# Kernel optimization log

Measured on AMD Instinct MI355X. Metric: run time of the kernel, lower is better.

Reference implementation:

```python
import jax, jax.numpy as jnp
import numpy as np

N_USERS = 50000
N_ENTITIES = 100000
D = 64
R = 16
E_UI = 1500000
E_KG = 100000


def setup_inputs() -> dict:
    key = jax.random.key(0)
    ks = jax.random.split(key, 7)
    s = 1.0 / np.sqrt(D)  # ~xavier scale
    return {
        "user_indices": jnp.arange(N_USERS, dtype=jnp.int32),
        "item_indices": jnp.arange(N_ENTITIES, dtype=jnp.int32),
        "edge_index_ui": jax.random.randint(ks[0], (2, E_UI), 0, N_USERS + N_ENTITIES, dtype=jnp.int32),
        "edge_index_kg": jax.random.randint(ks[1], (2, E_KG), 0, N_ENTITIES, dtype=jnp.int32),
        "edge_type_kg": jax.random.randint(ks[2], (E_KG,), 0, R, dtype=jnp.int32),
        "user_table": (jax.random.normal(ks[3], (N_USERS, D)) * s).astype(jnp.float32),
        "entity_table": (jax.random.normal(ks[4], (N_ENTITIES, D)) * s).astype(jnp.float32),
        "W": (jax.random.normal(ks[5], (D, D)) * s).astype(jnp.float32),
        "W_r": (jax.random.normal(ks[6], (R, D, D)) * s).astype(jnp.float32),
    }


def _kgat_layer(x, edge_index, W, W_r, edge_type=None):
    # PyG aggr='add', flow source_to_target: x_j = x[src], x_i = x[dst], scatter to dst
    src, dst = edge_index[0], edge_index[1]
    x_j = x[src]  # [E, D]
    x_i = x[dst]  # [E, D]
    if edge_type is None:
        x_j_t = x_j @ W  # [E, D]
    else:
        # per-edge relation-specific transform: bmm(x_j[:,None,:], W_r[edge_type])
        x_j_t = jnp.einsum('ed,edo->eo', x_j, W_r[edge_type])
    # bi-interaction attention
    x_i_t = x_i @ W
    logits = jnp.sum(x_i_t * x_j_t, axis=1, keepdims=True)  # [E, 1]
    logits = jax.nn.leaky_relu(logits, negative_slope=0.2)
    scores = jax.nn.softmax(logits, axis=0)  # GLOBAL softmax over all edges (as in source)
    msg = scores * x_j_t  # [E, D]
    return jax.ops.segment_sum(msg, dst, num_segments=x.shape[0])


def reference(user_indices, item_indices, edge_index_ui, edge_index_kg, edge_type_kg,
              user_table, entity_table, W, W_r):
    user_embeds = user_table[user_indices]      # [n_users, D]
    item_embeds = entity_table[item_indices]    # [n_entities, D]
    x = jnp.concatenate([user_embeds, item_embeds], axis=0)
    # single layer (layer_dims = [embed_dim])
    x_ui = _kgat_layer(x, edge_index_ui, W, W_r, edge_type=None)
    x_kg = _kgat_layer(item_embeds, edge_index_kg, W, W_r, edge_type=edge_type_kg)
    x = x.at[N_USERS:].add(x_kg)  # faithful to source: overwritten by next line (dead store)
    x = jax.nn.relu(x_ui)
    # F.dropout(training=False) -> identity in eval mode
    return (x[:N_USERS], x[N_USERS:])
```

## Files before the change

kernel.cpp:

```cpp
#include <hip/hip_runtime.h>

#define NU 50000
#define NE 100000
#define NN 150000
#define DD 64
#define EUI 1500000

#define TPB 256
#define NBLK 2048
#define NXB 2344
#define NXH (NXB + NBLK)
#define NBF2 9375
#define NSC 9375

#define XWB_OFF    0ull
#define CNT_OFF    4800000ull
#define PSUM_OFF   4950000ull
#define SCAL_OFF   4959375ull

__device__ __forceinline__ unsigned bfpack(float a, float b) {
  unsigned ua = __float_as_uint(a);
  ua = (ua + 0x7fffu + ((ua >> 16) & 1u)) >> 16;
  unsigned ub = __float_as_uint(b);
  ub = (ub + 0x7fffu + ((ub >> 16) & 1u)) & 0xffff0000u;
  return (ua & 0xffffu) | ub;
}

template <int CTRL>
__device__ __forceinline__ float dpp_add(float x) {
  int y = __builtin_amdgcn_update_dpp(0, __float_as_int(x), CTRL, 0xF, 0xF, false);
  return x + __int_as_float(y);
}
__device__ __forceinline__ float row16_sum(float x) {
  x = dpp_add<0x124>(x);
  x = dpp_add<0x128>(x);
  x = dpp_add<0xB1>(x);
  x = dpp_add<0x4E>(x);
  return x;
}

__global__ __launch_bounds__(TPB) void k_xw_hist(const int* __restrict__ uidx,
                                                 const int* __restrict__ iidx,
                                                 const float* __restrict__ ut,
                                                 const float* __restrict__ et,
                                                 const float* __restrict__ W,
                                                 unsigned* __restrict__ xwb,
                                                 const int* __restrict__ ei,
                                                 unsigned* __restrict__ cnt,
                                                 int* __restrict__ ssrcp) {
  const int bi = blockIdx.x;
  int idx;
  bool hist;
  if (bi < 2 * NBLK) { hist = (bi & 1); idx = bi >> 1; }
  else               { hist = false;    idx = bi - NBLK; }

  if (hist) {
    for (int e = idx * TPB + threadIdx.x; e < EUI; e += NBLK * TPB) {
      const int dst = ei[EUI + e];
      const int src = ei[e];
      const unsigned r = atomicAdd(&cnt[dst], 1u);
      if (r < 64u) ssrcp[((size_t)dst << 6) + r] = src;
    }
    return;
  }

  __shared__ float Ws[DD * DD];
  __shared__ float Xs[64 * 68];
  const int t = threadIdx.x;
  {
    const float4* W4 = (const float4*)W;
    float4* Ws4 = (float4*)Ws;
#pragma unroll
    for (int i = 0; i < 4; ++i) Ws4[t + i * TPB] = W4[t + i * TPB];
  }
  {
    const int rl = t >> 2, ch = t & 3;
    int row = idx * 64 + rl;
    if (row >= NN) row = NN - 1;
    const float4* s4 = (const float4*)((row < NU)
        ? ut + (size_t)uidx[row] * DD
        : et + (size_t)iidx[row - NU] * DD);
    float4* x4 = (float4*)(Xs + rl * 68);
#pragma unroll
    for (int j = 0; j < 4; ++j) x4[ch + 4 * j] = s4[ch + 4 * j];
  }
  __syncthreads();
  const int q = t & 15, g = t >> 4;
  float4 acc[4] = {{0,0,0,0},{0,0,0,0},{0,0,0,0},{0,0,0,0}};
  const float* __restrict__ wsq = Ws + 4 * q;
  const float* __restrict__ xsg = Xs + (4 * g) * 68;
#pragma unroll 1
  for (int kc = 0; kc < 16; ++kc) {
    const float4 w0 = *(const float4*)(wsq + (4 * kc + 0) * DD);
    const float4 w1 = *(const float4*)(wsq + (4 * kc + 1) * DD);
    const float4 w2 = *(const float4*)(wsq + (4 * kc + 2) * DD);
    const float4 w3 = *(const float4*)(wsq + (4 * kc + 3) * DD);
#pragma unroll
    for (int i = 0; i < 4; ++i) {
      const float4 x = *(const float4*)(xsg + i * 68 + 4 * kc);
      acc[i].x = fmaf(x.x, w0.x, acc[i].x);
      acc[i].y = fmaf(x.x, w0.y, acc[i].y);
      acc[i].z = fmaf(x.x, w0.z, acc[i].z);
      acc[i].w = fmaf(x.x, w0.w, acc[i].w);
      acc[i].x = fmaf(x.y, w1.x, acc[i].x);
      acc[i].y = fmaf(x.y, w1.y, acc[i].y);
      acc[i].z = fmaf(x.y, w1.z, acc[i].z);
      acc[i].w = fmaf(x.y, w1.w, acc[i].w);
      acc[i].x = fmaf(x.z, w2.x, acc[i].x);
      acc[i].y = fmaf(x.z, w2.y, acc[i].y);
      acc[i].z = fmaf(x.z, w2.z, acc[i].z);
      acc[i].w = fmaf(x.z, w2.w, acc[i].w);
      acc[i].x = fmaf(x.w, w3.x, acc[i].x);
      acc[i].y = fmaf(x.w, w3.y, acc[i].y);
      acc[i].z = fmaf(x.w, w3.z, acc[i].z);
      acc[i].w = fmaf(x.w, w3.w, acc[i].w);
    }
  }
#pragma unroll
  for (int i = 0; i < 4; ++i) {
    const int row = idx * 64 + 4 * g + i;
    if (row < NN) {
      uint2 p;
      p.x = bfpack(acc[i].x, acc[i].y);
      p.y = bfpack(acc[i].z, acc[i].w);
      ((uint2*)(xwb + (size_t)row * 32))[q] = p;
    }
  }
}

__global__ __launch_bounds__(TPB) void k_fused(const unsigned* __restrict__ cnt,
                                               const int* ssrcp,
                                               const unsigned* __restrict__ xwb,
                                               float* out,
                                               float* __restrict__ psum) {
  const int lane = threadIdx.x & 63;
  const int wv = threadIdx.x >> 6;
  const int sub = lane >> 4;
  const int q = lane & 15;
  const int n = blockIdx.x * 16 + wv * 4 + sub;
  const uint2* __restrict__ x2 = (const uint2*)xwb;
  const uint2 dv = x2[(size_t)n * 16 + q];
  const float vd0 = __uint_as_float(dv.x << 16);
  const float vd1 = __uint_as_float(dv.x & 0xffff0000u);
  const float vd2 = __uint_as_float(dv.y << 16);
  const float vd3 = __uint_as_float(dv.y & 0xffff0000u);
  const int deg = min((int)cnt[n], 64);
  const size_t base = (size_t)n << 6;
  float a0 = 0.f, a1 = 0.f, a2 = 0.f, a3 = 0.f, wacc = 0.f;
  for (int it = 0;; it += 2) {
    const bool act0 = it < deg;
    if (!__any(act0)) break;
    const bool act1 = it + 1 < deg;
    int s0 = ssrcp[base + (act0 ? it : 0)];
    int s1 = ssrcp[base + (act1 ? it + 1 : 0)];
    if (!act0) s0 = 0;
    if (!act1) s1 = 0;
    const uint2 sv0 = x2[(size_t)s0 * 16 + q];
    const uint2 sv1 = x2[(size_t)s1 * 16 + q];
    const float u0 = __uint_as_float(sv0.x << 16);
    const float u1 = __uint_as_float(sv0.x & 0xffff0000u);
    const float u2 = __uint_as_float(sv0.y << 16);
    const float u3 = __uint_as_float(sv0.y & 0xffff0000u);
    const float t0 = __uint_as_float(sv1.x << 16);
    const float t1 = __uint_as_float(sv1.x & 0xffff0000u);
    const float t2 = __uint_as_float(sv1.y << 16);
    const float t3 = __uint_as_float(sv1.y & 0xffff0000u);
    float p0 = vd0 * u0;
    p0 = fmaf(vd1, u1, p0);
    p0 = fmaf(vd2, u2, p0);
    p0 = fmaf(vd3, u3, p0);
    float p1 = vd0 * t0;
    p1 = fmaf(vd1, t1, p1);
    p1 = fmaf(vd2, t2, p1);
    p1 = fmaf(vd3, t3, p1);
    p0 = row16_sum(p0);
    p1 = row16_sum(p1);
    const float l0 = (p0 > 0.f) ? p0 : 0.2f * p0;
    const float l1 = (p1 > 0.f) ? p1 : 0.2f * p1;
    float w0 = __expf(l0);
    float w1 = __expf(l1);
    if (!act0) w0 = 0.f;
    if (!act1) w1 = 0.f;
    a0 = fmaf(w0, u0, a0);
    a1 = fmaf(w0, u1, a1);
    a2 = fmaf(w0, u2, a2);
    a3 = fmaf(w0, u3, a3);
    a0 = fmaf(w1, t0, a0);
    a1 = fmaf(w1, t1, a1);
    a2 = fmaf(w1, t2, a2);
    a3 = fmaf(w1, t3, a3);
    wacc += w0 + w1;
  }
  float4 r = {a0, a1, a2, a3};
  ((float4*)(out + (size_t)n * DD))[q] = r;
  __shared__ float sm[16];
  if (q == 0) sm[wv * 4 + sub] = wacc;
  __syncthreads();
  if (threadIdx.x == 0) {
    float s = 0.f;
#pragma unroll
    for (int i = 0; i < 16; ++i) s += sm[i];
    psum[blockIdx.x] = s;
  }
}

__global__ __launch_bounds__(TPB) void k_rsum(const float* __restrict__ psum,
                                              float* __restrict__ scal) {
  float s = 0.f;
  for (int i = threadIdx.x; i < NBF2; i += TPB) s += psum[i];
#pragma unroll
  for (int off = 32; off; off >>= 1) s += __shfl_xor(s, off, 64);
  __shared__ float sm[4];
  if ((threadIdx.x & 63) == 0) sm[threadIdx.x >> 6] = s;
  __syncthreads();
  if (threadIdx.x == 0) scal[0] = sm[0] + sm[1] + sm[2] + sm[3];
}

__global__ __launch_bounds__(TPB) void k_scale(float* __restrict__ out,
                                               const float* __restrict__ scal) {
  const float inv = 1.0f / scal[0];
  const int i = blockIdx.x * TPB + threadIdx.x;
  float4* o4 = (float4*)out;
  float4 v = o4[i];
  v.x = fmaxf(v.x * inv, 0.f);
  v.y = fmaxf(v.y * inv, 0.f);
  v.z = fmaxf(v.z * inv, 0.f);
  v.w = fmaxf(v.w * inv, 0.f);
  o4[i] = v;
}

extern "C" void kernel_launch(void* const* d_in, const int* in_sizes, int n_in,
                              void* d_out, int out_size, void* d_ws, size_t ws_size,
                              hipStream_t stream) {
  const int* uidx = (const int*)d_in[0];
  const int* iidx = (const int*)d_in[1];
  const int* ei_ui = (const int*)d_in[2];
  const float* ut = (const float*)d_in[5];
  const float* et = (const float*)d_in[6];
  const float* W = (const float*)d_in[7];

  float* out = (float*)d_out;
  float* ws = (float*)d_ws;
  unsigned* xwb = (unsigned*)(ws + XWB_OFF);
  unsigned* cnt = (unsigned*)(ws + CNT_OFF);
  float* psum = ws + PSUM_OFF;
  float* scal = ws + SCAL_OFF;
  int* ssrcp = (int*)d_out;

  (void)hipMemsetAsync(cnt, 0, (size_t)NN * sizeof(unsigned), stream);

  k_xw_hist<<<NXH, TPB, 0, stream>>>(uidx, iidx, ut, et, W, xwb, ei_ui, cnt, ssrcp);
  k_fused<<<NBF2, TPB, 0, stream>>>(cnt, ssrcp, xwb, out, psum);
  k_rsum<<<1, TPB, 0, stream>>>(psum, scal);
  k_scale<<<NSC, TPB, 0, stream>>>(out, scal);
}
```

Measured before the change: 255.3 us.

## Fuse aggregation, reduction and scaling into one persistent cooperative kernel

Replaces the three kernels (aggregation, softmax-denominator reduction, scale+ReLU) with one persistent cooperative kernel. Each block loops over tiles, folds its partial sum into a global atomic, waits at a grid-wide sync, then applies the normalisation and ReLU. The neighbour loop now uses a trip count shared by the wave and prefetches the next source indices. This removes two kernel launches and the partial-sum buffer, at the cost of a grid barrier and a fixed grid of 1024 blocks that may limit latency hiding.

```diff
diff --git a/kernel.cpp b/kernel.cpp
--- a/kernel.cpp
+++ b/kernel.cpp
@@ -1,4 +1,5 @@
 #include <hip/hip_runtime.h>
+#include <hip/hip_cooperative_groups.h>
 
 #define NU 50000
 #define NE 100000
@@ -11,12 +12,11 @@
 #define NXB 2344
 #define NXH (NXB + NBLK)
 #define NBF2 9375
-#define NSC 9375
+#define NPERS 1024
 
 #define XWB_OFF    0ull
 #define CNT_OFF    4800000ull
-#define PSUM_OFF   4950000ull
-#define SCAL_OFF   4959375ull
+#define SCAL_OFF   4950000ull
 
 __device__ __forceinline__ unsigned bfpack(float a, float b) {
   unsigned ua = __float_as_uint(a);
@@ -128,105 +128,110 @@
   }
 }
 
-__global__ __launch_bounds__(TPB) void k_fused(const unsigned* __restrict__ cnt,
-                                               const int* ssrcp,
-                                               const unsigned* __restrict__ xwb,
-                                               float* out,
-                                               float* __restrict__ psum) {
+__global__ __launch_bounds__(TPB) void k_fused_all(const unsigned* __restrict__ cnt,
+                                                   const int* ssrcp,
+                                                   const unsigned* __restrict__ xwb,
+                                                   float* out,
+                                                   float* scal) {
   const int lane = threadIdx.x & 63;
   const int wv = threadIdx.x >> 6;
   const int sub = lane >> 4;
   const int q = lane & 15;
-  const int n = blockIdx.x * 16 + wv * 4 + sub;
   const uint2* __restrict__ x2 = (const uint2*)xwb;
-  const uint2 dv = x2[(size_t)n * 16 + q];
-  const float vd0 = __uint_as_float(dv.x << 16);
-  const float vd1 = __uint_as_float(dv.x & 0xffff0000u);
-  const float vd2 = __uint_as_float(dv.y << 16);
-  const float vd3 = __uint_as_float(dv.y & 0xffff0000u);
-  const int deg = min((int)cnt[n], 64);
-  const size_t base = (size_t)n << 6;
-  float a0 = 0.f, a1 = 0.f, a2 = 0.f, a3 = 0.f, wacc = 0.f;
-  for (int it = 0;; it += 2) {
-    const bool act0 = it < deg;
-    if (!__any(act0)) break;
-    const bool act1 = it + 1 < deg;
-    int s0 = ssrcp[base + (act0 ? it : 0)];
-    int s1 = ssrcp[base + (act1 ? it + 1 : 0)];
-    if (!act0) s0 = 0;
-    if (!act1) s1 = 0;
-    const uint2 sv0 = x2[(size_t)s0 * 16 + q];
-    const uint2 sv1 = x2[(size_t)s1 * 16 + q];
-    const float u0 = __uint_as_float(sv0.x << 16);
-    const float u1 = __uint_as_float(sv0.x & 0xffff0000u);
-    const float u2 = __uint_as_float(sv0.y << 16);
-    const float u3 = __uint_as_float(sv0.y & 0xffff0000u);
-    const float t0 = __uint_as_float(sv1.x << 16);
-    const float t1 = __uint_as_float(sv1.x & 0xffff0000u);
-    const float t2 = __uint_as_float(sv1.y << 16);
-    const float t3 = __uint_as_float(sv1.y & 0xffff0000u);
-    float p0 = vd0 * u0;
-    p0 = fmaf(vd1, u1, p0);
-    p0 = fmaf(vd2, u2, p0);
-    p0 = fmaf(vd3, u3, p0);
-    float p1 = vd0 * t0;
-    p1 = fmaf(vd1, t1, p1);
-    p1 = fmaf(vd2, t2, p1);
-    p1 = fmaf(vd3, t3, p1);
-    p0 = row16_sum(p0);
-    p1 = row16_sum(p1);
-    const float l0 = (p0 > 0.f) ? p0 : 0.2f * p0;
-    const float l1 = (p1 > 0.f) ? p1 : 0.2f * p1;
-    float w0 = __expf(l0);
-    float w1 = __expf(l1);
-    if (!act0) w0 = 0.f;
-    if (!act1) w1 = 0.f;
-    a0 = fmaf(w0, u0, a0);
-    a1 = fmaf(w0, u1, a1);
-    a2 = fmaf(w0, u2, a2);
-    a3 = fmaf(w0, u3, a3);
-    a0 = fmaf(w1, t0, a0);
-    a1 = fmaf(w1, t1, a1);
-    a2 = fmaf(w1, t2, a2);
-    a3 = fmaf(w1, t3, a3);
-    wacc += w0 + w1;
-  }
-  float4 r = {a0, a1, a2, a3};
-  ((float4*)(out + (size_t)n * DD))[q] = r;
-  __shared__ float sm[16];
-  if (q == 0) sm[wv * 4 + sub] = wacc;
-  __syncthreads();
-  if (threadIdx.x == 0) {
-    float s = 0.f;
-#pragma unroll
-    for (int i = 0; i < 16; ++i) s += sm[i];
-    psum[blockIdx.x] = s;
-  }
-}
-
-__global__ __launch_bounds__(TPB) void k_rsum(const float* __restrict__ psum,
-                                              float* __restrict__ scal) {
-  float s = 0.f;
-  for (int i = threadIdx.x; i < NBF2; i += TPB) s += psum[i];
+  float wtot = 0.f;
+
+  for (int tile = blockIdx.x; tile < NBF2; tile += NPERS) {
+    const int n = tile * 16 + wv * 4 + sub;
+    const uint2 dv = x2[(size_t)n * 16 + q];
+    const float vd0 = __uint_as_float(dv.x << 16);
+    const float vd1 = __uint_as_float(dv.x & 0xffff0000u);
+    const float vd2 = __uint_as_float(dv.y << 16);
+    const float vd3 = __uint_as_float(dv.y & 0xffff0000u);
+    const int deg = min((int)cnt[n], 64);
+    int dmax = deg;
+    dmax = max(dmax, __shfl_xor(dmax, 16, 64));
+    dmax = max(dmax, __shfl_xor(dmax, 32, 64));
+    const size_t base = (size_t)n << 6;
+    const int nit = (dmax + 1) >> 1;
+    float a0 = 0.f, a1 = 0.f, a2 = 0.f, a3 = 0.f, wacc = 0.f;
+    int sl0 = ssrcp[base];
+    int sl1 = ssrcp[base + 1];
+    for (int ii = 0; ii < nit; ++ii) {
+      const int it = 2 * ii;
+      int s0 = sl0, s1 = sl1;
+      if (ii + 1 < nit) { sl0 = ssrcp[base + it + 2]; sl1 = ssrcp[base + it + 3]; }
+      const bool act0 = it < deg;
+      const bool act1 = it + 1 < deg;
+      if (!act0) s0 = 0;
+      if (!act1) s1 = 0;
+      const uint2 sv0 = x2[(size_t)s0 * 16 + q];
+      const uint2 sv1 = x2[(size_t)s1 * 16 + q];
+      const float u0 = __uint_as_float(sv0.x << 16);
+      const float u1 = __uint_as_float(sv0.x & 0xffff0000u);
+      const float u2 = __uint_as_float(sv0.y << 16);
+      const float u3 = __uint_as_float(sv0.y & 0xffff0000u);
+      const float t0 = __uint_as_float(sv1.x << 16);
+      const float t1 = __uint_as_float(sv1.x & 0xffff0000u);
+      const float t2 = __uint_as_float(sv1.y << 16);
+      const float t3 = __uint_as_float(sv1.y & 0xffff0000u);
+      float p0 = vd0 * u0;
+      p0 = fmaf(vd1, u1, p0);
+      p0 = fmaf(vd2, u2, p0);
+      p0 = fmaf(vd3, u3, p0);
+      float p1 = vd0 * t0;
+      p1 = fmaf(vd1, t1, p1);
+      p1 = fmaf(vd2, t2, p1);
+      p1 = fmaf(vd3, t3, p1);
+      p0 = row16_sum(p0);
+      p1 = row16_sum(p1);
+      const float l0 = (p0 > 0.f) ? p0 : 0.2f * p0;
+      const float l1 = (p1 > 0.f) ? p1 : 0.2f * p1;
+      float w0 = __expf(l0);
+      float w1 = __expf(l1);
+      if (!act0) w0 = 0.f;
+      if (!act1) w1 = 0.f;
+      a0 = fmaf(w0, u0, a0);
+      a1 = fmaf(w0, u1, a1);
+      a2 = fmaf(w0, u2, a2);
+      a3 = fmaf(w0, u3, a3);
+      a0 = fmaf(w1, t0, a0);
+      a1 = fmaf(w1, t1, a1);
+      a2 = fmaf(w1, t2, a2);
+      a3 = fmaf(w1, t3, a3);
+      wacc += w0 + w1;
+    }
+    float4 r = {a0, a1, a2, a3};
+    ((float4*)(out + (size_t)n * DD))[q] = r;
+    if (q == 0) wtot += wacc;
+  }
+
+  float s = wtot;
 #pragma unroll
   for (int off = 32; off; off >>= 1) s += __shfl_xor(s, off, 64);
   __shared__ float sm[4];
-  if ((threadIdx.x & 63) == 0) sm[threadIdx.x >> 6] = s;
+  __shared__ float shinv;
+  if (lane == 0) sm[wv] = s;
   __syncthreads();
-  if (threadIdx.x == 0) scal[0] = sm[0] + sm[1] + sm[2] + sm[3];
-}
-
-__global__ __launch_bounds__(TPB) void k_scale(float* __restrict__ out,
-                                               const float* __restrict__ scal) {
-  const float inv = 1.0f / scal[0];
-  const int i = blockIdx.x * TPB + threadIdx.x;
+  if (threadIdx.x == 0) atomicAdd(scal, sm[0] + sm[1] + sm[2] + sm[3]);
+
+  cooperative_groups::this_grid().sync();
+
+  if (threadIdx.x == 0)
+    shinv = 1.0f / __hip_atomic_load(scal, __ATOMIC_ACQUIRE,
+                                     __HIP_MEMORY_SCOPE_AGENT);
+  __syncthreads();
+  const float inv = shinv;
+
   float4* o4 = (float4*)out;
-  float4 v = o4[i];
-  v.x = fmaxf(v.x * inv, 0.f);
-  v.y = fmaxf(v.y * inv, 0.f);
-  v.z = fmaxf(v.z * inv, 0.f);
-  v.w = fmaxf(v.w * inv, 0.f);
-  o4[i] = v;
+  for (int tile = blockIdx.x; tile < NBF2; tile += NPERS) {
+    const size_t i = (size_t)tile * 256 + threadIdx.x;
+    float4 v = o4[i];
+    v.x = fmaxf(v.x * inv, 0.f);
+    v.y = fmaxf(v.y * inv, 0.f);
+    v.z = fmaxf(v.z * inv, 0.f);
+    v.w = fmaxf(v.w * inv, 0.f);
+    o4[i] = v;
+  }
 }
 
 extern "C" void kernel_launch(void* const* d_in, const int* in_sizes, int n_in,
@@ -243,14 +248,17 @@
   float* ws = (float*)d_ws;
   unsigned* xwb = (unsigned*)(ws + XWB_OFF);
   unsigned* cnt = (unsigned*)(ws + CNT_OFF);
-  float* psum = ws + PSUM_OFF;
   float* scal = ws + SCAL_OFF;
   int* ssrcp = (int*)d_out;
 
-  (void)hipMemsetAsync(cnt, 0, (size_t)NN * sizeof(unsigned), stream);
+  (void)hipMemsetAsync(cnt, 0, (size_t)(NN + 1) * sizeof(unsigned), stream);
 
   k_xw_hist<<<NXH, TPB, 0, stream>>>(uidx, iidx, ut, et, W, xwb, ei_ui, cnt, ssrcp);
-  k_fused<<<NBF2, TPB, 0, stream>>>(cnt, ssrcp, xwb, out, psum);
-  k_rsum<<<1, TPB, 0, stream>>>(psum, scal);
-  k_scale<<<NSC, TPB, 0, stream>>>(out, scal);
-}
+
+  {
+    void* args[] = {(void*)&cnt, (void*)&ssrcp, (void*)&xwb, (void*)&out,
+                    (void*)&scal};
+    (void)hipLaunchCooperativeKernel((const void*)k_fused_all, dim3(NPERS),
+                                     dim3(TPB), args, 0, stream);
+  }
+}
```

After: 431.4 us. 69.0% more time.
